# Optimization experiments

Hardware: AMD Instinct MI355X
Metric: run time of the kernel (lower is better)

Reference implementation:

```python
import jax, jax.numpy as jnp
import numpy as np

TGT, SRC, BATCH, HID, ATT = 64, 64, 32, 512, 512

def setup_inputs() -> dict:
    key = jax.random.key(0)
    k1, k2, k3, k4 = jax.random.split(key, 4)
    h_t = jax.random.normal(k1, (TGT, BATCH, HID), dtype=jnp.float32)
    src_encodings = jax.random.normal(k2, (SRC, BATCH, HID), dtype=jnp.float32)
    # Wa: Linear(2*HID -> ATT, bias=False); stored as (in, out) for jnp.
    Wa = jax.random.normal(k3, (2 * HID, ATT), dtype=jnp.float32) * (1.0 / np.sqrt(2 * HID))
    # Va: Linear(ATT -> 1, bias=False)
    Va = jax.random.normal(k4, (ATT,), dtype=jnp.float32) * (1.0 / np.sqrt(ATT))
    return {"h_t": h_t, "src_encodings": src_encodings, "Wa": Wa, "Va": Va}

def reference(h_t, src_encodings, Wa, Va):
    # Wa([h_t, src]) = h_t @ Wa_h + src @ Wa_s (exact by linearity of concat-matmul)
    Wa_h, Wa_s = Wa[:HID], Wa[HID:]                 # (H, A) each
    h_part = jnp.einsum('tbh,ha->tba', h_t, Wa_h)   # (T, B, A)
    s_part = jnp.einsum('sbh,ha->sba', src_encodings, Wa_s)  # (S, B, A)
    # scores[s, t, b] = Va . tanh(h_part[t,b] + s_part[s,b])
    hidden = jnp.tanh(h_part[None, :, :, :] + s_part[:, None, :, :])  # (S, T, B, A)
    scores = jnp.einsum('stba,a->stb', hidden, Va)  # (S, T, B)
    attn = jax.nn.softmax(scores, axis=0)           # softmax over src dim
    # context[t,b,:] = sum_s attn[s,t,b] * src[s,b,:]
    context = jnp.einsum('stb,sbh->tbh', attn, src_encodings)  # (T, B, H)
    return context
```

## Files before the change

kernel.cpp:

```cpp
#include <hip/hip_runtime.h>
#include <hip/hip_bf16.h>

#define TGT   64
#define SRCN  64
#define BATCH 32
#define HID   512
#define ATT   512
#define MROWS (TGT * BATCH)

typedef __bf16 bf16_t;
typedef __bf16 bf16x8 __attribute__((ext_vector_type(8)));
typedef float  f32x4  __attribute__((ext_vector_type(4)));

__device__ __forceinline__ float fast_exp2(float x) {
#if __has_builtin(__builtin_amdgcn_exp2f)
  return __builtin_amdgcn_exp2f(x);
#else
  float r; asm("v_exp_f32 %0, %1\n\ts_nop 1" : "=v"(r) : "v"(x)); return r;
#endif
}
__device__ __forceinline__ float fast_rcp(float x) {
#if __has_builtin(__builtin_amdgcn_rcpf)
  return __builtin_amdgcn_rcpf(x);
#else
  float r; asm("v_rcp_f32 %0, %1\n\ts_nop 1" : "=v"(r) : "v"(x)); return r;
#endif
}

#define MFMA(a, b, c) __builtin_amdgcn_mfma_f32_16x16x32_bf16((a), (b), (c), 0, 0, 0)

__global__ __launch_bounds__(256) void proj_gemm(
    const float* __restrict__ h_t, const float* __restrict__ srcp,
    const float* __restrict__ Wa, float* __restrict__ C)
{
  const int z = blockIdx.z;
  const float* __restrict__ A = z ? srcp : h_t;
  const int mbase = blockIdx.x * 64;
  const int nbase = blockIdx.y * 64;

  __shared__ bf16_t Ah[64][72];
  __shared__ bf16_t Al[64][72];
  __shared__ bf16_t Bh[64][72];
  __shared__ bf16_t Bl[64][72];

  const int tid  = threadIdx.x;
  const int lane = tid & 63;
  const int wv   = tid >> 6;
  const int wm   = (wv & 1) * 32;
  const int wn   = (wv >> 1) * 32;
  const int l15  = lane & 15;
  const int qd   = lane >> 4;

  const int arow = tid >> 2;
  const int akc  = (tid & 3) * 16;
  const int bn = tid & 63;
  const int bkg = (tid >> 6) * 16;

  const float* Aptr = A + (size_t)(mbase + arow) * HID + akc;
  const float* Bptr = Wa + (size_t)(z * HID + bkg) * ATT + nbase + bn;

  f32x4 acc00 = {0.f, 0.f, 0.f, 0.f};
  f32x4 acc01 = acc00, acc10 = acc00, acc11 = acc00;

  for (int kb = 0; kb < HID; kb += 64) {
    if (kb) __syncthreads();

    {
      float4 a0 = *(const float4*)(Aptr + kb);
      float4 a1 = *(const float4*)(Aptr + kb + 4);
      float4 a2 = *(const float4*)(Aptr + kb + 8);
      float4 a3 = *(const float4*)(Aptr + kb + 12);
      float av[16] = {a0.x, a0.y, a0.z, a0.w, a1.x, a1.y, a1.z, a1.w,
                      a2.x, a2.y, a2.z, a2.w, a3.x, a3.y, a3.z, a3.w};
      bf16x8 hi0, hi1, lo0, lo1;
#pragma unroll
      for (int j = 0; j < 8; ++j) {
        bf16_t h = (bf16_t)av[j];
        hi0[j] = h;
        lo0[j] = (bf16_t)(av[j] - (float)h);
        bf16_t h2 = (bf16_t)av[j + 8];
        hi1[j] = h2;
        lo1[j] = (bf16_t)(av[j + 8] - (float)h2);
      }
      *(bf16x8*)&Ah[arow][akc]     = hi0;
      *(bf16x8*)&Ah[arow][akc + 8] = hi1;
      *(bf16x8*)&Al[arow][akc]     = lo0;
      *(bf16x8*)&Al[arow][akc + 8] = lo1;
    }

    {
      const float* bp = Bptr + (size_t)kb * ATT;
      float bv[16];
#pragma unroll
      for (int j = 0; j < 16; ++j) bv[j] = bp[(size_t)j * ATT];
      bf16x8 hi0, hi1, lo0, lo1;
#pragma unroll
      for (int j = 0; j < 8; ++j) {
        bf16_t h = (bf16_t)bv[j];
        hi0[j] = h;
        lo0[j] = (bf16_t)(bv[j] - (float)h);
        bf16_t h2 = (bf16_t)bv[j + 8];
        hi1[j] = h2;
        lo1[j] = (bf16_t)(bv[j + 8] - (float)h2);
      }
      *(bf16x8*)&Bh[bn][bkg]     = hi0;
      *(bf16x8*)&Bh[bn][bkg + 8] = hi1;
      *(bf16x8*)&Bl[bn][bkg]     = lo0;
      *(bf16x8*)&Bl[bn][bkg + 8] = lo1;
    }
    __syncthreads();

#pragma unroll
    for (int h = 0; h < 2; ++h) {
      const int kh = h * 32 + qd * 8;
      bf16x8 ah0 = *(const bf16x8*)&Ah[wm + l15][kh];
      bf16x8 ah1 = *(const bf16x8*)&Ah[wm + 16 + l15][kh];
      bf16x8 al0 = *(const bf16x8*)&Al[wm + l15][kh];
      bf16x8 al1 = *(const bf16x8*)&Al[wm + 16 + l15][kh];
      bf16x8 bh0 = *(const bf16x8*)&Bh[wn + l15][kh];
      bf16x8 bh1 = *(const bf16x8*)&Bh[wn + 16 + l15][kh];
      bf16x8 bl0 = *(const bf16x8*)&Bl[wn + l15][kh];
      bf16x8 bl1 = *(const bf16x8*)&Bl[wn + 16 + l15][kh];

      acc00 = MFMA(ah0, bh0, acc00);
      acc01 = MFMA(ah0, bh1, acc01);
      acc10 = MFMA(ah1, bh0, acc10);
      acc11 = MFMA(ah1, bh1, acc11);
      acc00 = MFMA(al0, bh0, acc00);
      acc01 = MFMA(al0, bh1, acc01);
      acc10 = MFMA(al1, bh0, acc10);
      acc11 = MFMA(al1, bh1, acc11);
      acc00 = MFMA(ah0, bl0, acc00);
      acc01 = MFMA(ah0, bl1, acc01);
      acc10 = MFMA(ah1, bl0, acc10);
      acc11 = MFMA(ah1, bl1, acc11);
    }
  }

  float* Cz = C + (size_t)z * (MROWS * ATT);
#pragma unroll
  for (int r = 0; r < 4; ++r) {
    int row0 = mbase + wm + qd * 4 + r;
    int row1 = row0 + 16;
    int col0 = nbase + wn + l15;
    Cz[(size_t)row0 * ATT + col0]      = acc00[r];
    Cz[(size_t)row0 * ATT + col0 + 16] = acc01[r];
    Cz[(size_t)row1 * ATT + col0]      = acc10[r];
    Cz[(size_t)row1 * ATT + col0 + 16] = acc11[r];
  }
}

__global__ __launch_bounds__(512) void attn_fused(
    const float* __restrict__ ws, const float* __restrict__ srcp,
    const float* __restrict__ Va, float* __restrict__ out)
{
  const float* __restrict__ h_part = ws;
  const float* __restrict__ s_part = ws + (size_t)TGT * BATCH * ATT;
  const float SC = 2.8853900817779268f;

  const int t0   = blockIdx.x * 4;
  const int b    = blockIdx.y;
  const int tid  = threadIdx.x;
  const int lane = tid & 63;
  const int wv   = tid >> 6;

  __shared__ float scoreLds[4][64];
  __shared__ float attnLds[4][64];

  const int abase = lane * 8;
  float va[8], eH[4][8];
  *(float4*)&va[0] = *(const float4*)(Va + abase);
  *(float4*)&va[4] = *(const float4*)(Va + abase + 4);

  float vsum = 0.f;
#pragma unroll
  for (int j = 0; j < 8; ++j) vsum += va[j];
#pragma unroll
  for (int off = 32; off; off >>= 1) vsum += __shfl_xor(vsum, off);

#pragma unroll
  for (int t = 0; t < 4; ++t) {
    const float* hp = h_part + ((size_t)(t0 + t) * BATCH + b) * ATT + abase;
    float4 h0 = *(const float4*)hp;
    float4 h1 = *(const float4*)(hp + 4);
    float hv[8] = {h0.x, h0.y, h0.z, h0.w, h1.x, h1.y, h1.z, h1.w};
#pragma unroll
    for (int j = 0; j < 8; ++j) eH[t][j] = fast_exp2(hv[j] * SC);
  }

#pragma unroll 2
  for (int i = 0; i < 8; ++i) {
    const int s = wv * 8 + i;
    const float* sp = s_part + ((size_t)s * BATCH + b) * ATT + abase;
    float4 s0 = *(const float4*)sp;
    float4 s1 = *(const float4*)(sp + 4);
    float sv[8] = {s0.x, s0.y, s0.z, s0.w, s1.x, s1.y, s1.z, s1.w};
    float ex[8];
#pragma unroll
    for (int j = 0; j < 8; ++j) ex[j] = fast_exp2(sv[j] * SC);

    float q0 = 0.f, q1 = 0.f, q2 = 0.f, q3 = 0.f;
#pragma unroll
    for (int j = 0; j < 8; ++j) {
      float e = ex[j];
      float vj = va[j];
      float y0 = fmaf(e, eH[0][j], 1.0f);
      float y1 = fmaf(e, eH[1][j], 1.0f);
      float y2 = fmaf(e, eH[2][j], 1.0f);
      float y3 = fmaf(e, eH[3][j], 1.0f);
      float r01 = fast_rcp(y0 * y1);
      float r23 = fast_rcp(y2 * y3);
      q0 = fmaf(vj * y1, r01, q0);
      q1 = fmaf(vj * y0, r01, q1);
      q2 = fmaf(vj * y3, r23, q2);
      q3 = fmaf(vj * y2, r23, q3);
    }
#pragma unroll
    for (int off = 32; off; off >>= 1) {
      q0 += __shfl_xor(q0, off);
      q1 += __shfl_xor(q1, off);
      q2 += __shfl_xor(q2, off);
      q3 += __shfl_xor(q3, off);
    }
    if (lane == 0) {
      scoreLds[0][s] = vsum - 2.0f * q0;
      scoreLds[1][s] = vsum - 2.0f * q1;
      scoreLds[2][s] = vsum - 2.0f * q2;
      scoreLds[3][s] = vsum - 2.0f * q3;
    }
  }
  __syncthreads();

  if (wv < 4) {
    float sc = scoreLds[wv][lane];
    float m = sc;
#pragma unroll
    for (int off = 32; off; off >>= 1) m = fmaxf(m, __shfl_xor(m, off));
    float e = fast_exp2((sc - m) * 1.4426950408889634f);
    float ssum = e;
#pragma unroll
    for (int off = 32; off; off >>= 1) ssum += __shfl_xor(ssum, off);
    attnLds[wv][lane] = e * fast_rcp(ssum);
  }
  __syncthreads();

  {
    float c0 = 0.f, c1 = 0.f, c2 = 0.f, c3 = 0.f;
    const float* sb = srcp + (size_t)b * HID + tid;
#pragma unroll 8
    for (int s = 0; s < SRCN; ++s) {
      float sv = sb[(size_t)s * BATCH * HID];
      c0 = fmaf(attnLds[0][s], sv, c0);
      c1 = fmaf(attnLds[1][s], sv, c1);
      c2 = fmaf(attnLds[2][s], sv, c2);
      c3 = fmaf(attnLds[3][s], sv, c3);
    }
    out[((size_t)(t0 + 0) * BATCH + b) * HID + tid] = c0;
    out[((size_t)(t0 + 1) * BATCH + b) * HID + tid] = c1;
    out[((size_t)(t0 + 2) * BATCH + b) * HID + tid] = c2;
    out[((size_t)(t0 + 3) * BATCH + b) * HID + tid] = c3;
  }
}

extern "C" void kernel_launch(void* const* d_in, const int* in_sizes, int n_in,
                              void* d_out, int out_size, void* d_ws, size_t ws_size,
                              hipStream_t stream) {
  const float* h_t = (const float*)d_in[0];
  const float* src = (const float*)d_in[1];
  const float* Wa  = (const float*)d_in[2];
  const float* Va  = (const float*)d_in[3];
  float* out = (float*)d_out;
  float* C   = (float*)d_ws;

  proj_gemm<<<dim3(32, 8, 2), 256, 0, stream>>>(h_t, src, Wa, C);
  attn_fused<<<dim3(16, 32), 512, 0, stream>>>(C, src, Va, out);
}
```

Measured before the change: 97.48 us.

## Prefetch GEMM tiles, precompute exponentials in GEMM epilogue, merge score reductions

The projection GEMM now loads the next K-slice of A and Wa into registers while MFMAs run on the current slice, overlapping global loads with compute. The GEMM epilogue stores exp2(2x*log2e) instead of the raw projections, so the attention kernel no longer recomputes exponentials for every (t,s) pair. The four per-target score reductions are packed into a single butterfly using lane-half swaps, cutting the shuffle count. The cost is extra live registers in the GEMM and a small exp cost in its epilogue.

Result: faster. 95.44 us (-2.1%).

```diff
diff --git a/kernel.cpp b/kernel.cpp
--- a/kernel.cpp
+++ b/kernel.cpp
@@ -28,6 +28,8 @@
 }
 
 #define MFMA(a, b, c) __builtin_amdgcn_mfma_f32_16x16x32_bf16((a), (b), (c), 0, 0, 0)
+
+#define SC_EXP 2.8853900817779268f
 
 __global__ __launch_bounds__(256) void proj_gemm(
     const float* __restrict__ h_t, const float* __restrict__ srcp,
@@ -62,16 +64,20 @@
   f32x4 acc00 = {0.f, 0.f, 0.f, 0.f};
   f32x4 acc01 = acc00, acc10 = acc00, acc11 = acc00;
 
+  float4 pa0 = *(const float4*)(Aptr);
+  float4 pa1 = *(const float4*)(Aptr + 4);
+  float4 pa2 = *(const float4*)(Aptr + 8);
+  float4 pa3 = *(const float4*)(Aptr + 12);
+  float pb[16];
+#pragma unroll
+  for (int j = 0; j < 16; ++j) pb[j] = Bptr[(size_t)j * ATT];
+
   for (int kb = 0; kb < HID; kb += 64) {
     if (kb) __syncthreads();
 
     {
-      float4 a0 = *(const float4*)(Aptr + kb);
-      float4 a1 = *(const float4*)(Aptr + kb + 4);
-      float4 a2 = *(const float4*)(Aptr + kb + 8);
-      float4 a3 = *(const float4*)(Aptr + kb + 12);
-      float av[16] = {a0.x, a0.y, a0.z, a0.w, a1.x, a1.y, a1.z, a1.w,
-                      a2.x, a2.y, a2.z, a2.w, a3.x, a3.y, a3.z, a3.w};
+      float av[16] = {pa0.x, pa0.y, pa0.z, pa0.w, pa1.x, pa1.y, pa1.z, pa1.w,
+                      pa2.x, pa2.y, pa2.z, pa2.w, pa3.x, pa3.y, pa3.z, pa3.w};
       bf16x8 hi0, hi1, lo0, lo1;
 #pragma unroll
       for (int j = 0; j < 8; ++j) {
@@ -89,19 +95,15 @@
     }
 
     {
-      const float* bp = Bptr + (size_t)kb * ATT;
-      float bv[16];
-#pragma unroll
-      for (int j = 0; j < 16; ++j) bv[j] = bp[(size_t)j * ATT];
       bf16x8 hi0, hi1, lo0, lo1;
 #pragma unroll
       for (int j = 0; j < 8; ++j) {
-        bf16_t h = (bf16_t)bv[j];
+        bf16_t h = (bf16_t)pb[j];
         hi0[j] = h;
-        lo0[j] = (bf16_t)(bv[j] - (float)h);
-        bf16_t h2 = (bf16_t)bv[j + 8];
+        lo0[j] = (bf16_t)(pb[j] - (float)h);
+        bf16_t h2 = (bf16_t)pb[j + 8];
         hi1[j] = h2;
-        lo1[j] = (bf16_t)(bv[j + 8] - (float)h2);
+        lo1[j] = (bf16_t)(pb[j + 8] - (float)h2);
       }
       *(bf16x8*)&Bh[bn][bkg]     = hi0;
       *(bf16x8*)&Bh[bn][bkg + 8] = hi1;
@@ -109,6 +111,17 @@
       *(bf16x8*)&Bl[bn][bkg + 8] = lo1;
     }
     __syncthreads();
+
+    const int kn = kb + 64;
+    if (kn < HID) {
+      pa0 = *(const float4*)(Aptr + kn);
+      pa1 = *(const float4*)(Aptr + kn + 4);
+      pa2 = *(const float4*)(Aptr + kn + 8);
+      pa3 = *(const float4*)(Aptr + kn + 12);
+      const float* bp = Bptr + (size_t)kn * ATT;
+#pragma unroll
+      for (int j = 0; j < 16; ++j) pb[j] = bp[(size_t)j * ATT];
+    }
 
 #pragma unroll
     for (int h = 0; h < 2; ++h) {
@@ -143,10 +156,10 @@
     int row0 = mbase + wm + qd * 4 + r;
     int row1 = row0 + 16;
     int col0 = nbase + wn + l15;
-    Cz[(size_t)row0 * ATT + col0]      = acc00[r];
-    Cz[(size_t)row0 * ATT + col0 + 16] = acc01[r];
-    Cz[(size_t)row1 * ATT + col0]      = acc10[r];
-    Cz[(size_t)row1 * ATT + col0 + 16] = acc11[r];
+    Cz[(size_t)row0 * ATT + col0]      = fast_exp2(acc00[r] * SC_EXP);
+    Cz[(size_t)row0 * ATT + col0 + 16] = fast_exp2(acc01[r] * SC_EXP);
+    Cz[(size_t)row1 * ATT + col0]      = fast_exp2(acc10[r] * SC_EXP);
+    Cz[(size_t)row1 * ATT + col0 + 16] = fast_exp2(acc11[r] * SC_EXP);
   }
 }
 
@@ -154,9 +167,8 @@
     const float* __restrict__ ws, const float* __restrict__ srcp,
     const float* __restrict__ Va, float* __restrict__ out)
 {
-  const float* __restrict__ h_part = ws;
-  const float* __restrict__ s_part = ws + (size_t)TGT * BATCH * ATT;
-  const float SC = 2.8853900817779268f;
+  const float* __restrict__ eh_part = ws;
+  const float* __restrict__ es_part = ws + (size_t)TGT * BATCH * ATT;
 
   const int t0   = blockIdx.x * 4;
   const int b    = blockIdx.y;
@@ -180,24 +192,21 @@
 
 #pragma unroll
   for (int t = 0; t < 4; ++t) {
-    const float* hp = h_part + ((size_t)(t0 + t) * BATCH + b) * ATT + abase;
-    float4 h0 = *(const float4*)hp;
-    float4 h1 = *(const float4*)(hp + 4);
-    float hv[8] = {h0.x, h0.y, h0.z, h0.w, h1.x, h1.y, h1.z, h1.w};
-#pragma unroll
-    for (int j = 0; j < 8; ++j) eH[t][j] = fast_exp2(hv[j] * SC);
-  }
+    const float* hp = eh_part + ((size_t)(t0 + t) * BATCH + b) * ATT + abase;
+    *(float4*)&eH[t][0] = *(const float4*)hp;
+    *(float4*)&eH[t][4] = *(const float4*)(hp + 4);
+  }
+
+  const bool hi32 = (lane & 32) != 0;
+  const bool hi16 = (lane & 16) != 0;
 
 #pragma unroll 2
   for (int i = 0; i < 8; ++i) {
     const int s = wv * 8 + i;
-    const float* sp = s_part + ((size_t)s * BATCH + b) * ATT + abase;
-    float4 s0 = *(const float4*)sp;
-    float4 s1 = *(const float4*)(sp + 4);
-    float sv[8] = {s0.x, s0.y, s0.z, s0.w, s1.x, s1.y, s1.z, s1.w};
+    const float* sp = es_part + ((size_t)s * BATCH + b) * ATT + abase;
     float ex[8];
-#pragma unroll
-    for (int j = 0; j < 8; ++j) ex[j] = fast_exp2(sv[j] * SC);
+    *(float4*)&ex[0] = *(const float4*)sp;
+    *(float4*)&ex[4] = *(const float4*)(sp + 4);
 
     float q0 = 0.f, q1 = 0.f, q2 = 0.f, q3 = 0.f;
 #pragma unroll
@@ -215,19 +224,21 @@
       q2 = fmaf(vj * y3, r23, q2);
       q3 = fmaf(vj * y2, r23, q3);
     }
-#pragma unroll
-    for (int off = 32; off; off >>= 1) {
-      q0 += __shfl_xor(q0, off);
-      q1 += __shfl_xor(q1, off);
-      q2 += __shfl_xor(q2, off);
-      q3 += __shfl_xor(q3, off);
-    }
-    if (lane == 0) {
-      scoreLds[0][s] = vsum - 2.0f * q0;
-      scoreLds[1][s] = vsum - 2.0f * q1;
-      scoreLds[2][s] = vsum - 2.0f * q2;
-      scoreLds[3][s] = vsum - 2.0f * q3;
-    }
+
+    float a02 = hi32 ? q2 : q0;
+    float b02 = hi32 ? q0 : q2;
+    float a13 = hi32 ? q3 : q1;
+    float b13 = hi32 ? q1 : q3;
+    a02 += __shfl_xor(b02, 32);
+    a13 += __shfl_xor(b13, 32);
+    float x = hi16 ? a13 : a02;
+    float y = hi16 ? a02 : a13;
+    x += __shfl_xor(y, 16);
+    x += __shfl_xor(x, 8);
+    x += __shfl_xor(x, 4);
+    x += __shfl_xor(x, 2);
+    x += __shfl_xor(x, 1);
+    if ((lane & 15) == 0) scoreLds[lane >> 4][s] = vsum - 2.0f * x;
   }
   __syncthreads();
 
```
